# Optimization experiments

Hardware: AMD Instinct MI355X
Metric: run time of the kernel (lower is better)

## Reference

```python
import jax, jax.numpy as jnp
import numpy as np

EMBED_DIM = 1024
NUM_HEADS = 16
HEAD_DIM = EMBED_DIM // NUM_HEADS


def setup_inputs() -> dict:
    key = jax.random.key(0)
    ks = jax.random.split(key, 5)
    s = 0.02
    return {
        "x": jax.random.normal(ks[0], (2, 2048, EMBED_DIM), dtype=jnp.float32),
        "w_qkv": jax.random.normal(ks[1], (EMBED_DIM, 3 * EMBED_DIM), dtype=jnp.float32) * s,
        "b_qkv": jnp.zeros((3 * EMBED_DIM,), dtype=jnp.float32),
        "w_out": jax.random.normal(ks[2], (EMBED_DIM, EMBED_DIM), dtype=jnp.float32) * s,
        "b_out": jnp.zeros((EMBED_DIM,), dtype=jnp.float32),
    }


def reference(x, w_qkv, b_qkv, w_out, b_out):
    B, T, C = x.shape
    qkv = x @ w_qkv + b_qkv                       # [B,T,3C]
    q, k, v = jnp.split(qkv, 3, axis=-1)
    # [B,T,C] -> [B,H,T,Dh]
    def heads(t):
        return t.reshape(B, T, NUM_HEADS, HEAD_DIM).transpose(0, 2, 1, 3)
    q, k, v = heads(q), heads(k), heads(v)
    scale = 1.0 / np.sqrt(HEAD_DIM).astype(np.float32)
    scores = jnp.einsum("bhqd,bhkd->bhqk", q, k) * scale  # [B,H,T,T]
    causal = jnp.tril(jnp.ones((T, T), dtype=bool))
    scores = jnp.where(causal[None, None], scores, -jnp.inf)
    attn = jax.nn.softmax(scores, axis=-1)
    out = jnp.einsum("bhqk,bhkd->bhqd", attn, v)  # [B,H,T,Dh]
    out = out.transpose(0, 2, 1, 3).reshape(B, T, C)
    return out @ w_out + b_out
```

## Files before the change

kernel.cpp:

```cpp
#include <hip/hip_runtime.h>

typedef unsigned short u16;
typedef unsigned int u32;
typedef __attribute__((ext_vector_type(8))) short bf16x8;
typedef __attribute__((ext_vector_type(4))) float f32x4;
typedef __attribute__((ext_vector_type(16))) float f32x16;

#define TOK   4096
#define EMB   1024
#define NQKV  3072
#define TSEQ  2048
#define NH    16

__device__ __forceinline__ u16 f2b(float f) {
  union { float f; unsigned u; } v; v.f = f;
  unsigned r = v.u + 0x7FFFu + ((v.u >> 16) & 1u);
  return (u16)(r >> 16);
}

__device__ __forceinline__ u32 pack_rn(float a, float b) {
  u32 ua = __float_as_uint(a) + 0x8000u;
  u32 ub = __float_as_uint(b) + 0x8000u;
  return __builtin_amdgcn_perm(ub, ua, 0x07060302u);
}

__device__ __forceinline__ f32x16 zero16() {
  f32x16 z;
#pragma unroll
  for (int i = 0; i < 16; i++) z[i] = 0.f;
  return z;
}

__device__ __forceinline__ void gload16(const void* g, void* l) {
  __builtin_amdgcn_global_load_lds((const __attribute__((address_space(1))) void*)g,
                                   (__attribute__((address_space(3))) void*)l, 16, 0, 0);
}


__global__ __launch_bounds__(256) void prep_kernel(const float* __restrict__ x,
                                                   u16* __restrict__ x_bf,
                                                   const float* __restrict__ w_qkv,
                                                   u16* __restrict__ wqkvT,
                                                   const float* __restrict__ w_out,
                                                   u16* __restrict__ woutT) {
  __shared__ u16 sm[64][65];
  int bid = blockIdx.x, tid = threadIdx.x;
  if (bid < 4096) {
    int i = bid * 256 + tid;
    float4 v = ((const float4*)x)[i];
    union { u16 us[4]; uint2 u2; } o;
    o.us[0] = f2b(v.x); o.us[1] = f2b(v.y); o.us[2] = f2b(v.z); o.us[3] = f2b(v.w);
    ((uint2*)x_bf)[i] = o.u2;
    return;
  }
  const float* src; u16* dst; int R, C, bx, by;
  if (bid < 4096 + 768) {
    int t = bid - 4096; bx = t % 48; by = t / 48;
    src = w_qkv; dst = wqkvT; R = EMB; C = NQKV;
  } else {
    int t = bid - 4096 - 768; bx = t & 15; by = t >> 4;
    src = w_out; dst = woutT; R = EMB; C = EMB;
  }
  int c0 = bx * 64, r0 = by * 64;
#pragma unroll
  for (int i = 0; i < 16; i++) {
    int idx = tid + i * 256;
    int r = idx >> 6, c = idx & 63;
    sm[r][c] = f2b(src[(size_t)(r0 + r) * C + c0 + c]);
  }
  __syncthreads();
#pragma unroll
  for (int i = 0; i < 16; i++) {
    int idx = tid + i * 256;
    int cc = idx >> 6, rr = idx & 63;
    dst[(size_t)(c0 + cc) * R + r0 + rr] = sm[rr][cc];
  }
}

__global__ __launch_bounds__(256) void transpose_v(const u16* __restrict__ V,
                                                   u16* __restrict__ Vt) {
  __shared__ u16 sm[64][72];
  int t0 = blockIdx.x * 64, bh = blockIdx.y;
  size_t base = (size_t)bh * TSEQ * 64;
  int tid = threadIdx.x;
  int r = tid >> 2, c = (tid & 3) * 16;
  *(bf16x8*)&sm[r][c]     = *(const bf16x8*)&V[base + (size_t)(t0 + r) * 64 + c];
  *(bf16x8*)&sm[r][c + 8] = *(const bf16x8*)&V[base + (size_t)(t0 + r) * 64 + c + 8];
  __syncthreads();
  int d = tid >> 2, tc = (tid & 3) * 16;
  union { u16 us[16]; uint4 v4[2]; } o;
#pragma unroll
  for (int i = 0; i < 16; i++) o.us[i] = sm[tc + i][d];
  *(uint4*)&Vt[base + (size_t)d * TSEQ + t0 + tc]     = o.v4[0];
  *(uint4*)&Vt[base + (size_t)d * TSEQ + t0 + tc + 8] = o.v4[1];
}


template <int MODE>
__global__ __launch_bounds__(256) void gemm_bt(const u16* __restrict__ A,
                                               const u16* __restrict__ Bt,
                                               const float* __restrict__ bias,
                                               u16* __restrict__ qb, u16* __restrict__ kb,
                                               u16* __restrict__ vb, float* __restrict__ outp,
                                               int K, int N) {
  __shared__ u16 As[2][128][64];
  __shared__ u16 Bs[2][128][64];
  int tid = threadIdx.x;
  int m0 = blockIdx.y * 128, n0 = blockIdx.x * 128;
  int lane = tid & 63, wid = tid >> 6;
  int wm = (wid >> 1) * 64;
  int wn = (wid & 1) * 64;
  int l15 = lane & 15, quad = lane >> 4;
  int srow = lane >> 3;
  int scol = (((lane & 7) ^ srow) * 8);

  f32x4 acc[4][4];
#pragma unroll
  for (int i = 0; i < 4; i++)
#pragma unroll
    for (int j = 0; j < 4; j++) acc[i][j] = (f32x4){0.f, 0.f, 0.f, 0.f};

  const u16* Ag = A + (size_t)(m0 + wid * 32 + srow) * K + scol;
  const u16* Bg = Bt + (size_t)(n0 + wid * 32 + srow) * K + scol;

#pragma unroll
  for (int i = 0; i < 4; i++)
    gload16(Ag + (size_t)(i * 8) * K, &As[0][wid * 32 + i * 8][0]);
#pragma unroll
  for (int i = 0; i < 4; i++)
    gload16(Bg + (size_t)(i * 8) * K, &Bs[0][wid * 32 + i * 8][0]);
  __syncthreads();

  int cur = 0;
  for (int k0 = 0; k0 < K; k0 += 64) {
    if (k0 + 64 < K) {
      int kn = k0 + 64;
#pragma unroll
      for (int i = 0; i < 4; i++)
        gload16(Ag + (size_t)(i * 8) * K + kn, &As[cur ^ 1][wid * 32 + i * 8][0]);
#pragma unroll
      for (int i = 0; i < 4; i++)
        gload16(Bg + (size_t)(i * 8) * K + kn, &Bs[cur ^ 1][wid * 32 + i * 8][0]);
    }

#pragma unroll
    for (int ks = 0; ks < 2; ks++) {
      bf16x8 af[4], bfr[4];
#pragma unroll
      for (int rt = 0; rt < 4; rt++)
        af[rt] = *(const bf16x8*)&As[cur][wm + rt * 16 + l15][((ks * 4 + quad) ^ (l15 & 7)) * 8];
#pragma unroll
      for (int ct = 0; ct < 4; ct++)
        bfr[ct] = *(const bf16x8*)&Bs[cur][wn + ct * 16 + l15][((ks * 4 + quad) ^ (l15 & 7)) * 8];
#pragma unroll
      for (int rt = 0; rt < 4; rt++)
#pragma unroll
        for (int ct = 0; ct < 4; ct++)
          acc[rt][ct] = __builtin_amdgcn_mfma_f32_16x16x32_bf16(bfr[ct], af[rt], acc[rt][ct], 0, 0, 0);
    }
    __syncthreads();
    cur ^= 1;
  }

#pragma unroll
  for (int rt = 0; rt < 4; rt++) {
#pragma unroll
    for (int ct = 0; ct < 4; ct++) {
      int m = m0 + wm + rt * 16 + l15;
      int nb = n0 + wn + ct * 16 + quad * 4;
      float4 b4 = *(const float4*)&bias[nb];
      float v0 = acc[rt][ct][0] + b4.x, v1 = acc[rt][ct][1] + b4.y;
      float v2 = acc[rt][ct][2] + b4.z, v3 = acc[rt][ct][3] + b4.w;
      if (MODE == 0) {
        int sel = nb >> 10;
        int c = nb & 1023;
        int h = c >> 6, d0 = c & 63;
        int b = m >> 11, t = m & 2047;
        u16* dst = (sel == 0) ? qb : (sel == 1) ? kb : vb;
        union { u32 u[2]; uint2 u2; } o;
        o.u[0] = pack_rn(v0, v1);
        o.u[1] = pack_rn(v2, v3);
        *(uint2*)&dst[((((size_t)b * NH + h) * TSEQ + t) << 6) + d0] = o.u2;
      } else {
        float4 o = {v0, v1, v2, v3};
        *(float4*)&outp[(size_t)m * N + nb] = o;
      }
    }
  }
}


__global__ __launch_bounds__(256, 4) void attn_kernel(const u16* __restrict__ Qb,
                                                      const u16* __restrict__ Kb,
                                                      const u16* __restrict__ Vtb,
                                                      u16* __restrict__ O) {
  __shared__ u16 Ks[64][68];
  __shared__ u16 Vt[64][68];
  __shared__ float Cmb[2][16][64][2];
  __shared__ float Lmb[2][32];

  const float SCL = 0.18033688f;
  const float MOFF = 16.0f;

  int id = blockIdx.x;
  int bh = (id >> 5) & 31;
  int q5 = id & 31;
  int qt = ((id >> 8) & 1) ? (31 - q5) : q5;

  int tid = threadIdx.x, lane = tid & 63, w = tid >> 6;
  int sub = w & 1, par = w >> 1;
  int l31 = lane & 31, h = lane >> 5;
  const size_t hoff = (size_t)bh * TSEQ * 64;

  int qw = qt * 64 + sub * 32;
  int qg = qw + l31;

  bf16x8 qf[4];
  {
    const u16* qp = Qb + hoff + (size_t)qg * 64 + h * 8;
#pragma unroll
    for (int s = 0; s < 4; s++) qf[s] = *(const bf16x8*)(qp + s * 16);
  }

  f32x16 acc[2];
  acc[0] = zero16(); acc[1] = zero16();
  float l_i = 0.f;

  int r = tid >> 2, cb = (tid & 3) * 16;
  bf16x8 kr0, kr1, vr0, vr1;
  {
    const u16* kg = Kb + hoff + (size_t)r * 64 + cb;
    const u16* vg = Vtb + hoff + (size_t)r * TSEQ + cb;
    kr0 = *(const bf16x8*)kg;       kr1 = *(const bf16x8*)(kg + 8);
    vr0 = *(const bf16x8*)vg;       vr1 = *(const bf16x8*)(vg + 8);
  }

  for (int kt = 0; kt <= qt; kt++) {
    __syncthreads();
    *(bf16x8*)&Ks[r][cb]     = kr0;
    *(bf16x8*)&Ks[r][cb + 8] = kr1;
    *(bf16x8*)&Vt[r][cb]     = vr0;
    *(bf16x8*)&Vt[r][cb + 8] = vr1;
    __syncthreads();
    if (kt < qt) {
      const u16* kg = Kb + hoff + (size_t)((kt + 1) * 64 + r) * 64 + cb;
      const u16* vg = Vtb + hoff + (size_t)r * TSEQ + (kt + 1) * 64 + cb;
      kr0 = *(const bf16x8*)kg;     kr1 = *(const bf16x8*)(kg + 8);
      vr0 = *(const bf16x8*)vg;     vr1 = *(const bf16x8*)(vg + 8);
    }

    int kbt = kt * 64 + par * 32;
    if (kbt <= qw + 31) {
      f32x16 sacc = zero16();
#pragma unroll
      for (int s = 0; s < 4; s++) {
        bf16x8 kf = *(const bf16x8*)&Ks[par * 32 + l31][s * 16 + h * 8];
        sacc = __builtin_amdgcn_mfma_f32_32x32x16_bf16(kf, qf[s], sacc, 0, 0, 0);
      }

      if (kbt + 31 > qw) {
#pragma unroll
        for (int rr = 0; rr < 16; rr++) {
          int key = kbt + (rr & 3) + 8 * (rr >> 2) + 4 * h;
          if (key > qg) sacc[rr] = -1e30f;
        }
      }

#pragma unroll
      for (int rr = 0; rr < 16; rr++) {
        float p = exp2f(__builtin_fmaf(sacc[rr], SCL, -MOFF));
        sacc[rr] = p;
        l_i += p;
      }

#pragma unroll
      for (int s2 = 0; s2 < 2; s2++) {
        u32 u0 = pack_rn(sacc[8 * s2 + 0], sacc[8 * s2 + 1]);
        u32 u1 = pack_rn(sacc[8 * s2 + 2], sacc[8 * s2 + 3]);
        u32 u2 = pack_rn(sacc[8 * s2 + 4], sacc[8 * s2 + 5]);
        u32 u3 = pack_rn(sacc[8 * s2 + 6], sacc[8 * s2 + 7]);
        u32 s0 = h ? u0 : u2, s1 = h ? u1 : u3;
        u32 t0 = (u32)__shfl_xor((int)s0, 32);
        u32 t1 = (u32)__shfl_xor((int)s1, 32);
        union { u32 d[4]; bf16x8 v; } pf;
        pf.d[0] = h ? t0 : u0;
        pf.d[1] = h ? t1 : u1;
        pf.d[2] = h ? u2 : t0;
        pf.d[3] = h ? u3 : t1;
#pragma unroll
        for (int dt = 0; dt < 2; dt++) {
          bf16x8 vf = *(const bf16x8*)&Vt[dt * 32 + l31][par * 32 + s2 * 16 + h * 8];
          acc[dt] = __builtin_amdgcn_mfma_f32_32x32x16_bf16(vf, pf.v, acc[dt], 0, 0, 0);
        }
      }
    }
  }

  l_i += __shfl_xor(l_i, 32);

  __syncthreads();
  if (par == 1) {
#pragma unroll
    for (int dt = 0; dt < 2; dt++)
#pragma unroll
      for (int pr = 0; pr < 8; pr++) {
        Cmb[sub][dt * 8 + pr][lane][0] = acc[dt][2 * pr];
        Cmb[sub][dt * 8 + pr][lane][1] = acc[dt][2 * pr + 1];
      }
    if (h == 0) Lmb[sub][l31] = l_i;
  }
  __syncthreads();
  if (par == 0) {
#pragma unroll
    for (int dt = 0; dt < 2; dt++)
#pragma unroll
      for (int pr = 0; pr < 8; pr++) {
        acc[dt][2 * pr]     += Cmb[sub][dt * 8 + pr][lane][0];
        acc[dt][2 * pr + 1] += Cmb[sub][dt * 8 + pr][lane][1];
      }
    float lt = l_i + Lmb[sub][l31];
    float inv = 1.0f / lt;

    int b = bh >> 4, head = bh & 15;
    size_t rowbase = ((size_t)b * TSEQ + qg) * 1024 + head * 64;
#pragma unroll
    for (int dt = 0; dt < 2; dt++)
#pragma unroll
      for (int G = 0; G < 4; G++) {
        union { u32 u[2]; uint2 u2; } o;
        o.u[0] = pack_rn(acc[dt][4 * G + 0] * inv, acc[dt][4 * G + 1] * inv);
        o.u[1] = pack_rn(acc[dt][4 * G + 2] * inv, acc[dt][4 * G + 3] * inv);
        *(uint2*)&O[rowbase + dt * 32 + G * 8 + 4 * h] = o.u2;
      }
  }
}


extern "C" void kernel_launch(void* const* d_in, const int* in_sizes, int n_in,
                              void* d_out, int out_size, void* d_ws, size_t ws_size,
                              hipStream_t stream) {
  (void)in_sizes; (void)n_in; (void)out_size; (void)ws_size;
  const float* x     = (const float*)d_in[0];
  const float* w_qkv = (const float*)d_in[1];
  const float* b_qkv = (const float*)d_in[2];
  const float* w_out = (const float*)d_in[3];
  const float* b_out = (const float*)d_in[4];
  float* out = (float*)d_out;

  char* p = (char*)d_ws;
  u16* x_bf  = (u16*)p; p += (size_t)TOK * EMB * 2;
  u16* wqkvT = (u16*)p; p += (size_t)NQKV * EMB * 2;
  u16* woutT = (u16*)p; p += (size_t)EMB * EMB * 2;
  u16* Qb    = (u16*)p; p += (size_t)32 * TSEQ * 64 * 2;
  u16* Kb    = (u16*)p; p += (size_t)32 * TSEQ * 64 * 2;
  u16* Vraw  = (u16*)p; p += (size_t)32 * TSEQ * 64 * 2;
  u16* attn_o = (u16*)p;
  u16* Vtb   = x_bf;

  prep_kernel<<<dim3(4096 + 768 + 256), 256, 0, stream>>>(x, x_bf, w_qkv, wqkvT, w_out, woutT);
  gemm_bt<0><<<dim3(NQKV / 128, TOK / 128), 256, 0, stream>>>(x_bf, wqkvT, b_qkv,
                                                              Qb, Kb, Vraw, nullptr, EMB, NQKV);
  transpose_v<<<dim3(TSEQ / 64, 32), 256, 0, stream>>>(Vraw, Vtb);
  attn_kernel<<<dim3(1024), 256, 0, stream>>>(Qb, Kb, Vtb, attn_o);
  gemm_bt<1><<<dim3(EMB / 128, TOK / 128), 256, 0, stream>>>(attn_o, woutT, b_out,
                                                             nullptr, nullptr, nullptr, out, EMB, EMB);
}
```

Baseline: 200.0 us.

## Use narrower N tiles for output GEMM and remap attention blocks per XCD

Templates the GEMM on the N tile width and launches the output projection with 64-wide tiles, doubling its block count to 512 so more CUs are busy on the 4096x1024 GEMM. Separately, the attention kernel's block-to-work mapping is changed so that consecutive physical block IDs, which are dealt round-robin across the 8 XCDs, keep each head's query tiles on one XCD for L2 reuse of K/V, with causal load balanced by reversing tile order for odd slots. The narrower tile lowers per-block arithmetic intensity, and the remap relies on the assumed round-robin dispatch order.

```diff
diff --git a/kernel.cpp b/kernel.cpp
--- a/kernel.cpp
+++ b/kernel.cpp
@@ -96,39 +96,41 @@
 }
 
 
-template <int MODE>
+template <int MODE, int TN>
 __global__ __launch_bounds__(256) void gemm_bt(const u16* __restrict__ A,
                                                const u16* __restrict__ Bt,
                                                const float* __restrict__ bias,
                                                u16* __restrict__ qb, u16* __restrict__ kb,
                                                u16* __restrict__ vb, float* __restrict__ outp,
                                                int K, int N) {
+  constexpr int CT = TN / 32;
+  constexpr int RB = TN / 32;
   __shared__ u16 As[2][128][64];
-  __shared__ u16 Bs[2][128][64];
+  __shared__ u16 Bs[2][TN][64];
   int tid = threadIdx.x;
-  int m0 = blockIdx.y * 128, n0 = blockIdx.x * 128;
+  int m0 = blockIdx.y * 128, n0 = blockIdx.x * TN;
   int lane = tid & 63, wid = tid >> 6;
   int wm = (wid >> 1) * 64;
-  int wn = (wid & 1) * 64;
+  int wn = (wid & 1) * (TN / 2);
   int l15 = lane & 15, quad = lane >> 4;
   int srow = lane >> 3;
   int scol = (((lane & 7) ^ srow) * 8);
 
-  f32x4 acc[4][4];
+  f32x4 acc[4][CT];
 #pragma unroll
   for (int i = 0; i < 4; i++)
 #pragma unroll
-    for (int j = 0; j < 4; j++) acc[i][j] = (f32x4){0.f, 0.f, 0.f, 0.f};
+    for (int j = 0; j < CT; j++) acc[i][j] = (f32x4){0.f, 0.f, 0.f, 0.f};
 
   const u16* Ag = A + (size_t)(m0 + wid * 32 + srow) * K + scol;
-  const u16* Bg = Bt + (size_t)(n0 + wid * 32 + srow) * K + scol;
+  const u16* Bg = Bt + (size_t)(n0 + wid * (TN / 4) + srow) * K + scol;
 
 #pragma unroll
   for (int i = 0; i < 4; i++)
     gload16(Ag + (size_t)(i * 8) * K, &As[0][wid * 32 + i * 8][0]);
 #pragma unroll
-  for (int i = 0; i < 4; i++)
-    gload16(Bg + (size_t)(i * 8) * K, &Bs[0][wid * 32 + i * 8][0]);
+  for (int i = 0; i < RB; i++)
+    gload16(Bg + (size_t)(i * 8) * K, &Bs[0][wid * (TN / 4) + i * 8][0]);
   __syncthreads();
 
   int cur = 0;
@@ -139,23 +141,23 @@
       for (int i = 0; i < 4; i++)
         gload16(Ag + (size_t)(i * 8) * K + kn, &As[cur ^ 1][wid * 32 + i * 8][0]);
 #pragma unroll
-      for (int i = 0; i < 4; i++)
-        gload16(Bg + (size_t)(i * 8) * K + kn, &Bs[cur ^ 1][wid * 32 + i * 8][0]);
+      for (int i = 0; i < RB; i++)
+        gload16(Bg + (size_t)(i * 8) * K + kn, &Bs[cur ^ 1][wid * (TN / 4) + i * 8][0]);
     }
 
 #pragma unroll
     for (int ks = 0; ks < 2; ks++) {
-      bf16x8 af[4], bfr[4];
+      bf16x8 af[4], bfr[CT];
 #pragma unroll
       for (int rt = 0; rt < 4; rt++)
         af[rt] = *(const bf16x8*)&As[cur][wm + rt * 16 + l15][((ks * 4 + quad) ^ (l15 & 7)) * 8];
 #pragma unroll
-      for (int ct = 0; ct < 4; ct++)
+      for (int ct = 0; ct < CT; ct++)
         bfr[ct] = *(const bf16x8*)&Bs[cur][wn + ct * 16 + l15][((ks * 4 + quad) ^ (l15 & 7)) * 8];
 #pragma unroll
       for (int rt = 0; rt < 4; rt++)
 #pragma unroll
-        for (int ct = 0; ct < 4; ct++)
+        for (int ct = 0; ct < CT; ct++)
           acc[rt][ct] = __builtin_amdgcn_mfma_f32_16x16x32_bf16(bfr[ct], af[rt], acc[rt][ct], 0, 0, 0);
     }
     __syncthreads();
@@ -165,7 +167,7 @@
 #pragma unroll
   for (int rt = 0; rt < 4; rt++) {
 #pragma unroll
-    for (int ct = 0; ct < 4; ct++) {
+    for (int ct = 0; ct < CT; ct++) {
       int m = m0 + wm + rt * 16 + l15;
       int nb = n0 + wn + ct * 16 + quad * 4;
       float4 b4 = *(const float4*)&bias[nb];
@@ -202,10 +204,12 @@
   const float SCL = 0.18033688f;
   const float MOFF = 16.0f;
 
-  int id = blockIdx.x;
-  int bh = (id >> 5) & 31;
-  int q5 = id & 31;
-  int qt = ((id >> 8) & 1) ? (31 - q5) : q5;
+  int phys = blockIdx.x;
+  int xcd = phys & 7;
+  int cuL = (phys >> 3) & 31;
+  int slot = phys >> 8;
+  int bh = xcd * 4 + slot;
+  int qt = (slot & 1) ? (31 - cuL) : cuL;
 
   int tid = threadIdx.x, lane = tid & 63, w = tid >> 6;
   int sub = w & 1, par = w >> 1;
@@ -358,10 +362,10 @@
   u16* Vtb   = x_bf;
 
   prep_kernel<<<dim3(4096 + 768 + 256), 256, 0, stream>>>(x, x_bf, w_qkv, wqkvT, w_out, woutT);
-  gemm_bt<0><<<dim3(NQKV / 128, TOK / 128), 256, 0, stream>>>(x_bf, wqkvT, b_qkv,
-                                                              Qb, Kb, Vraw, nullptr, EMB, NQKV);
+  gemm_bt<0, 128><<<dim3(NQKV / 128, TOK / 128), 256, 0, stream>>>(x_bf, wqkvT, b_qkv,
+                                                                   Qb, Kb, Vraw, nullptr, EMB, NQKV);
   transpose_v<<<dim3(TSEQ / 64, 32), 256, 0, stream>>>(Vraw, Vtb);
   attn_kernel<<<dim3(1024), 256, 0, stream>>>(Qb, Kb, Vtb, attn_o);
-  gemm_bt<1><<<dim3(EMB / 128, TOK / 128), 256, 0, stream>>>(attn_o, woutT, b_out,
-                                                             nullptr, nullptr, nullptr, out, EMB, EMB);
-}
+  gemm_bt<1, 64><<<dim3(EMB / 64, TOK / 128), 256, 0, stream>>>(attn_o, woutT, b_out,
+                                                                nullptr, nullptr, nullptr, out, EMB, EMB);
+}
```

New measurement: 195.6 us. 1.02x faster.
